# Kernel optimization log

Measured on AMD Instinct MI355X. Metric: run time of the kernel, lower is better.

The kernel has to match this reference:

```python
import jax, jax.numpy as jnp
import numpy as np

D_MODEL = 512
D_STATE = 16
D_CONV = 4
EXPAND = 2
D_INNER = EXPAND * D_MODEL          # 1024
DT_RANK = (D_MODEL + 15) // 16      # 32
B, L = 32, 2048
EPS = 1e-12


def _ln(x, g, b):
    mu = jnp.mean(x, axis=-1, keepdims=True)
    var = jnp.mean(jnp.square(x - mu), axis=-1, keepdims=True)
    return (x - mu) * jax.lax.rsqrt(var + EPS) * g + b


def setup_inputs() -> dict:
    key = jax.random.key(0)
    ks = jax.random.split(key, 12)
    s = lambda fan: 1.0 / np.sqrt(fan)
    inp = {
        "input_tensor": jax.random.normal(ks[0], (B, L, D_MODEL), jnp.float32),
        # Mamba params
        "in_proj_w": jax.random.normal(ks[1], (2 * D_INNER, D_MODEL), jnp.float32) * s(D_MODEL),
        "conv_w": jax.random.normal(ks[2], (D_INNER, D_CONV), jnp.float32) * s(D_CONV),
        "conv_b": jnp.zeros((D_INNER,), jnp.float32),
        "x_proj_w": jax.random.normal(ks[3], (DT_RANK + 2 * D_STATE, D_INNER), jnp.float32) * s(D_INNER),
        "dt_proj_w": jax.random.normal(ks[4], (D_INNER, DT_RANK), jnp.float32) * s(DT_RANK),
        "dt_proj_b": jnp.full((D_INNER,), -4.0, jnp.float32),  # softplus(-4) ~ small dt
        "A_log": jnp.log(jnp.broadcast_to(jnp.arange(1, D_STATE + 1, dtype=jnp.float32), (D_INNER, D_STATE))),
        "D": jnp.ones((D_INNER,), jnp.float32),
        "out_proj_w": jax.random.normal(ks[5], (D_MODEL, D_INNER), jnp.float32) * s(D_INNER),
        # block params
        "ln1_g": jnp.ones((D_MODEL,), jnp.float32),
        "ln1_b": jnp.zeros((D_MODEL,), jnp.float32),
        "w1_w": jax.random.normal(ks[6], (4 * D_MODEL, D_MODEL), jnp.float32) * s(D_MODEL),
        "w1_b": jnp.zeros((4 * D_MODEL,), jnp.float32),
        "w2_w": jax.random.normal(ks[7], (D_MODEL, 4 * D_MODEL), jnp.float32) * s(4 * D_MODEL),
        "w2_b": jnp.zeros((D_MODEL,), jnp.float32),
        "ln2_g": jnp.ones((D_MODEL,), jnp.float32),
        "ln2_b": jnp.zeros((D_MODEL,), jnp.float32),
    }
    return inp


def _mamba(x, in_proj_w, conv_w, conv_b, x_proj_w, dt_proj_w, dt_proj_b, A_log, D, out_proj_w):
    # x: [B, L, d_model]
    xz = jnp.einsum("bld,ed->ble", x, in_proj_w)          # [B,L,2*d_inner]
    xi, z = jnp.split(xz, 2, axis=-1)                      # each [B,L,d_inner]

    # depthwise causal conv1d along L (d_conv taps)
    xpad = jnp.pad(xi, ((0, 0), (D_CONV - 1, 0), (0, 0)))
    conv = conv_b
    for k in range(D_CONV):
        conv = conv + xpad[:, k:k + L, :] * conv_w[:, k]
    u = jax.nn.silu(conv)                                  # [B,L,d_inner]

    # input-dependent dt, B, C
    x_dbl = jnp.einsum("bld,ed->ble", u, x_proj_w)         # [B,L,dt_rank+2N]
    dt, B_t, C_t = jnp.split(x_dbl, [DT_RANK, DT_RANK + D_STATE], axis=-1)
    delta = jax.nn.softplus(jnp.einsum("blr,dr->bld", dt, dt_proj_w) + dt_proj_b)  # [B,L,d_inner]

    A = -jnp.exp(A_log)                                    # [d_inner, N]

    def step(h, inp):
        u_t, d_t, Bt, Ct = inp                             # [B,d_in],[B,d_in],[B,N],[B,N]
        dA = jnp.exp(d_t[..., None] * A)                   # [B,d_in,N]
        h = h * dA + (d_t * u_t)[..., None] * Bt[:, None, :]
        y = jnp.sum(h * Ct[:, None, :], axis=-1)           # [B,d_in]
        return h, y

    h0 = jnp.zeros((B, D_INNER, D_STATE), u.dtype)
    xs = (jnp.swapaxes(u, 0, 1), jnp.swapaxes(delta, 0, 1),
          jnp.swapaxes(B_t, 0, 1), jnp.swapaxes(C_t, 0, 1))
    _, ys = jax.lax.scan(step, h0, xs)                     # [L,B,d_inner]
    y = jnp.swapaxes(ys, 0, 1) + u * D
    y = y * jax.nn.silu(z)
    return jnp.einsum("ble,de->bld", y, out_proj_w)        # [B,L,d_model]


def reference(input_tensor, in_proj_w, conv_w, conv_b, x_proj_w, dt_proj_w, dt_proj_b,
              A_log, D, out_proj_w, ln1_g, ln1_b, w1_w, w1_b, w2_w, w2_b, ln2_g, ln2_b):
    h = _mamba(input_tensor, in_proj_w, conv_w, conv_b, x_proj_w, dt_proj_w,
               dt_proj_b, A_log, D, out_proj_w)
    h = _ln(h + input_tensor, ln1_g, ln1_b)                # num_layers > 1 branch, dropout=0
    f = jax.nn.gelu(jnp.einsum("bld,fd->blf", h, w1_w) + w1_b, approximate=False)
    f = jnp.einsum("blf,df->bld", f, w2_w) + w2_b
    return _ln(f + h, ln2_g, ln2_b)
```

## Files before the change

kernel.cpp:

```cpp
#include <hip/hip_runtime.h>
#include <hip/hip_bf16.h>

#define DM 512
#define DI 1024
#define DC 4
#define DTR 32
#define NST 16
#define LSEQ 2048
#define NBATCH 32
#define NCH 16
#define CHL 128

typedef __attribute__((ext_vector_type(8))) short b16x8;
typedef __attribute__((ext_vector_type(4))) float fx4;
typedef __attribute__((ext_vector_type(4))) unsigned short u16x4;

__device__ __forceinline__ unsigned short f2bf(float f) {
    union { float f; unsigned u; } x; x.f = f;
    unsigned r = x.u + 0x7fffu + ((x.u >> 16) & 1u);
    return (unsigned short)(r >> 16);
}
__device__ __forceinline__ float bf2f(unsigned short u) {
    union { unsigned u; float f; } x; x.u = ((unsigned)u) << 16;
    return x.f;
}

__global__ __launch_bounds__(256) void cast_kernel(const float* __restrict__ src,
                                                   unsigned short* __restrict__ dst, int n4) {
    int i = blockIdx.x * 256 + threadIdx.x;
    if (i < n4) {
        fx4 v = *(const fx4*)&src[(size_t)i * 4];
        u16x4 o;
        #pragma unroll
        for (int j = 0; j < 4; j++) o[j] = f2bf(v[j]);
        *(u16x4*)&dst[(size_t)i * 4] = o;
    }
}

__global__ __launch_bounds__(256) void extract_dt_kernel(const float* __restrict__ xdbl,
                                                         unsigned short* __restrict__ dt16) {
    int i = blockIdx.x * 256 + threadIdx.x;
    int m = i >> 5, r = i & 31;
    dt16[i] = f2bf(xdbl[(size_t)m * 64 + r]);
}

template <int BN, int EPI, bool HAS_BIAS>
__global__ __launch_bounds__(256, 2) void gemm_bf16(const unsigned short* __restrict__ A,
                                                    const unsigned short* __restrict__ W,
                                                    const float* __restrict__ bias,
                                                    void* __restrict__ Cout, int N, int K) {
    constexpr int BM = 128, BK = 32;
    __shared__ __align__(16) unsigned short As[BM * BK];
    __shared__ __align__(16) unsigned short Ws[BN * BK];
    const int tid = threadIdx.x;
    const int wave = tid >> 6, lane = tid & 63;
    const int lr = lane & 15, lg = lane >> 4;
    const int m0 = blockIdx.y * BM, n0 = blockIdx.x * BN;
    const int wm0 = (wave >> 1) * 64, wn0 = (wave & 1) * (BN / 2);
    constexpr int NR = BN / 32;
    fx4 acc[4][NR];
    #pragma unroll
    for (int i = 0; i < 4; i++)
        #pragma unroll
        for (int j = 0; j < NR; j++) acc[i][j] = fx4{0.f, 0.f, 0.f, 0.f};

    for (int k0 = 0; k0 < K; k0 += BK) {
        #pragma unroll
        for (int i = 0; i < (BM * BK / 8) / 256; i++) {
            int cb = (i * 4 + wave) * 64, c = cb + lane;
            int row = c >> 2, kk = (c & 3) * 8;
            const unsigned short* g = A + (size_t)(m0 + row) * K + k0 + kk;
            __builtin_amdgcn_global_load_lds(
                (const __attribute__((address_space(1))) unsigned int*)g,
                (__attribute__((address_space(3))) unsigned int*)&As[cb * 8], 16, 0, 0);
        }
        #pragma unroll
        for (int i = 0; i < (BN * BK / 8) / 256; i++) {
            int cb = (i * 4 + wave) * 64, c = cb + lane;
            int row = c >> 2, kk = (c & 3) * 8;
            const unsigned short* g = W + (size_t)(n0 + row) * K + k0 + kk;
            __builtin_amdgcn_global_load_lds(
                (const __attribute__((address_space(1))) unsigned int*)g,
                (__attribute__((address_space(3))) unsigned int*)&Ws[cb * 8], 16, 0, 0);
        }
        __syncthreads();
        b16x8 af[4], bfr[NR];
        #pragma unroll
        for (int mi = 0; mi < 4; mi++)
            af[mi] = *(const b16x8*)&As[(wm0 + mi * 16 + lr) * BK + lg * 8];
        #pragma unroll
        for (int ni = 0; ni < NR; ni++)
            bfr[ni] = *(const b16x8*)&Ws[(wn0 + ni * 16 + lr) * BK + lg * 8];
        #pragma unroll
        for (int mi = 0; mi < 4; mi++)
            #pragma unroll
            for (int ni = 0; ni < NR; ni++)
                acc[mi][ni] = __builtin_amdgcn_mfma_f32_16x16x32_bf16(af[mi], bfr[ni],
                                                                     acc[mi][ni], 0, 0, 0);
        __syncthreads();
    }
    #pragma unroll
    for (int mi = 0; mi < 4; mi++) {
        #pragma unroll
        for (int ni = 0; ni < NR; ni++) {
            #pragma unroll
            for (int j2 = 0; j2 < 4; j2++) {
                int row = m0 + wm0 + mi * 16 + lg * 4 + j2;
                int col = n0 + wn0 + ni * 16 + lr;
                float v = acc[mi][ni][j2];
                if (HAS_BIAS) v += bias[col];
                size_t o = (size_t)row * N + col;
                if (EPI == 0) {
                    ((float*)Cout)[o] = v;
                } else if (EPI == 1) {
                    ((unsigned short*)Cout)[o] = f2bf(v);
                } else if (EPI == 2) {
                    v = 0.5f * v * (1.f + erff(v * 0.70710678118654752f));
                    ((unsigned short*)Cout)[o] = f2bf(v);
                } else if (EPI == 3) {
                    v = (v > 20.f) ? v : log1pf(__expf(v));
                    ((float*)Cout)[o] = v;
                } else {
                    v = (v > 20.f) ? v : log1pf(__expf(v));
                    ((unsigned short*)Cout)[o] = f2bf(v);
                }
            }
        }
    }
}

__global__ __launch_bounds__(256) void conv_silu_kernel(const unsigned short* __restrict__ xz16,
                                                        const float* __restrict__ cw,
                                                        const float* __restrict__ cb,
                                                        unsigned short* __restrict__ u16) {
    int idx = blockIdx.x * 256 + threadIdx.x;
    int m = idx >> 7;
    int d0 = (idx & 127) << 3;
    int l = m & (LSEQ - 1);
    float acc[8];
    fx4 w0[8];
    #pragma unroll
    for (int j = 0; j < 8; j++) {
        acc[j] = cb[d0 + j];
        w0[j] = *(const fx4*)&cw[(d0 + j) * 4];
    }
    #pragma unroll
    for (int k = 0; k < 4; k++) {
        int lm = l - 3 + k;
        if (lm >= 0) {
            b16x8 xv = *(const b16x8*)&xz16[(size_t)(m - 3 + k) * (2 * DI) + d0];
            #pragma unroll
            for (int j = 0; j < 8; j++) acc[j] += bf2f((unsigned short)xv[j]) * w0[j][k];
        }
    }
    b16x8 o;
    #pragma unroll
    for (int j = 0; j < 8; j++) {
        float v = acc[j];
        v = v / (1.f + __expf(-v));
        o[j] = (short)f2bf(v);
    }
    *(b16x8*)&u16[(size_t)m * DI + d0] = o;
}

__device__ __forceinline__ bool load_A(const float* __restrict__ A_log, int d, float* Av) {
    bool fast = true;
    #pragma unroll
    for (int n = 0; n < NST; n++) {
        Av[n] = -__expf(A_log[(size_t)d * NST + n]);
        fast = fast && (fabsf(Av[n] + (float)(n + 1)) < 1e-4f * (float)(n + 1));
    }
    return fast;
}

__global__ __launch_bounds__(256) void scan_partial(const unsigned short* __restrict__ delta16,
                                                    const unsigned short* __restrict__ u16,
                                                    const float* __restrict__ xdbl,
                                                    const float* __restrict__ A_log,
                                                    float* __restrict__ sumd,
                                                    float* __restrict__ hend) {
    int d = blockIdx.x * 256 + threadIdx.x;
    int ch = blockIdx.y, b = blockIdx.z;
    size_t bL = (size_t)b * LSEQ + (size_t)ch * CHL;
    float Av[NST], h[NST];
    const bool fast = load_A(A_log, d, Av);
    #pragma unroll
    for (int n = 0; n < NST; n++) h[n] = 0.f;
    float S = 0.f;
    __shared__ float bs[8][16];
    for (int l0 = 0; l0 < CHL; l0 += 8) {
        __syncthreads();
        if (threadIdx.x < 128) {
            int j = threadIdx.x >> 4, c = threadIdx.x & 15;
            bs[j][c] = xdbl[(bL + l0 + j) * 64 + 32 + c];
        }
        __syncthreads();
        #pragma unroll
        for (int jj = 0; jj < 8; jj++) {
            size_t r = bL + l0 + jj;
            float dl = bf2f(delta16[r * DI + d]);
            float uu = bf2f(u16[r * DI + d]);
            S += dl;
            float du = dl * uu;
            if (fast) {
                float e1 = __expf(-dl), en = 1.f;
                #pragma unroll
                for (int n = 0; n < NST; n++) {
                    en *= e1;
                    h[n] = h[n] * en + du * bs[jj][n];
                }
            } else {
                #pragma unroll
                for (int n = 0; n < NST; n++)
                    h[n] = h[n] * __expf(dl * Av[n]) + du * bs[jj][n];
            }
        }
    }
    size_t base = ((size_t)(b * NCH + ch) * NST) * DI + d;
    #pragma unroll
    for (int n = 0; n < NST; n++) hend[base + (size_t)n * DI] = h[n];
    sumd[(size_t)(b * NCH + ch) * DI + d] = S;
}

__global__ __launch_bounds__(256) void scan_carry(const float* __restrict__ sumd,
                                                  const float* __restrict__ hend,
                                                  const float* __restrict__ A_log,
                                                  float* __restrict__ hin) {
    int d = blockIdx.x * 256 + threadIdx.x;
    int b = blockIdx.y;
    float Av[NST], h[NST];
    #pragma unroll
    for (int n = 0; n < NST; n++) {
        Av[n] = -__expf(A_log[(size_t)d * NST + n]);
        h[n] = 0.f;
    }
    for (int k = 0; k < NCH; k++) {
        size_t base = ((size_t)(b * NCH + k) * NST) * DI + d;
        float S = sumd[(size_t)(b * NCH + k) * DI + d];
        #pragma unroll
        for (int n = 0; n < NST; n++) {
            hin[base + (size_t)n * DI] = h[n];
            h[n] = h[n] * __expf(S * Av[n]) + hend[base + (size_t)n * DI];
        }
    }
}

__global__ __launch_bounds__(256) void scan_final(const unsigned short* __restrict__ delta16,
                                                  const unsigned short* u16,
                                                  const unsigned short* __restrict__ xz16,
                                                  const float* __restrict__ xdbl,
                                                  const float* __restrict__ A_log,
                                                  const float* __restrict__ Dp,
                                                  const float* __restrict__ hin,
                                                  unsigned short* y16) {
    int d = blockIdx.x * 256 + threadIdx.x;
    int ch = blockIdx.y, b = blockIdx.z;
    size_t bL = (size_t)b * LSEQ + (size_t)ch * CHL;
    float Av[NST], h[NST];
    const bool fast = load_A(A_log, d, Av);
    size_t base = ((size_t)(b * NCH + ch) * NST) * DI + d;
    #pragma unroll
    for (int n = 0; n < NST; n++) h[n] = hin[base + (size_t)n * DI];
    float Dd = Dp[d];
    __shared__ float bc[8][32];
    for (int l0 = 0; l0 < CHL; l0 += 8) {
        __syncthreads();
        {
            int j = threadIdx.x >> 5, c = threadIdx.x & 31;
            bc[j][c] = xdbl[(bL + l0 + j) * 64 + 32 + c];
        }
        __syncthreads();
        #pragma unroll
        for (int jj = 0; jj < 8; jj++) {
            size_t r = bL + l0 + jj;
            float dl = bf2f(delta16[r * DI + d]);
            float uu = bf2f(u16[r * DI + d]);
            float zz = bf2f(xz16[r * (2 * DI) + DI + d]);
            float du = dl * uu;
            float y = 0.f;
            if (fast) {
                float e1 = __expf(-dl), en = 1.f;
                #pragma unroll
                for (int n = 0; n < NST; n++) {
                    en *= e1;
                    h[n] = h[n] * en + du * bc[jj][n];
                    y += h[n] * bc[jj][16 + n];
                }
            } else {
                #pragma unroll
                for (int n = 0; n < NST; n++) {
                    h[n] = h[n] * __expf(dl * Av[n]) + du * bc[jj][n];
                    y += h[n] * bc[jj][16 + n];
                }
            }
            y = (y + uu * Dd) * (zz / (1.f + __expf(-zz)));
            y16[r * DI + d] = f2bf(y);
        }
        __syncthreads();
    }
}

__global__ __launch_bounds__(256) void ln_kernel(const float* __restrict__ a,
                                                 const float* __restrict__ res,
                                                 const float* __restrict__ g,
                                                 const float* __restrict__ bta,
                                                 float* __restrict__ out32,
                                                 unsigned short* __restrict__ out16) {
    int row = blockIdx.x, tid = threadIdx.x;
    size_t base = (size_t)row * DM;
    float v0 = a[base + tid] + res[base + tid];
    float v1 = a[base + tid + 256] + res[base + tid + 256];
    float s = v0 + v1, q = v0 * v0 + v1 * v1;
    #pragma unroll
    for (int m = 32; m >= 1; m >>= 1) {
        s += __shfl_xor(s, m);
        q += __shfl_xor(q, m);
    }
    __shared__ float rs[4], rq[4];
    int wv = tid >> 6;
    if ((tid & 63) == 0) { rs[wv] = s; rq[wv] = q; }
    __syncthreads();
    s = rs[0] + rs[1] + rs[2] + rs[3];
    q = rq[0] + rq[1] + rq[2] + rq[3];
    float mu = s * (1.f / DM);
    float var = q * (1.f / DM) - mu * mu;
    float rsg = rsqrtf(var + 1e-12f);
    float o0 = (v0 - mu) * rsg * g[tid] + bta[tid];
    float o1 = (v1 - mu) * rsg * g[tid + 256] + bta[tid + 256];
    out32[base + tid] = o0;
    out32[base + tid + 256] = o1;
    if (out16) {
        out16[base + tid] = f2bf(o0);
        out16[base + tid + 256] = f2bf(o1);
    }
}

static size_t align256(size_t b) { return (b + 255) & ~(size_t)255; }

static size_t tier_need(size_t Gb) {
    size_t R = Gb * LSEQ;
    size_t w = 0;
    w += align256((size_t)2 * DI * DM * 2);
    w += align256((size_t)64 * DI * 2);
    w += align256((size_t)DM * DI * 2);
    w += align256((size_t)4 * DM * DM * 2);
    w += align256((size_t)DM * 4 * DM * 2);
    w += align256((size_t)DI * DTR * 2);
    w += align256(R * 2048 * 2);
    w += align256(R * 1024 * 2);
    w += align256(R * 1024 * 4);
    w += align256(R * 64 * 4);
    w += align256(R * 32 * 2);
    w += align256(R * 512 * 2);
    w += align256(Gb * NCH * DI * 4);
    w += align256(Gb * NCH * NST * DI * 4);
    w += align256(Gb * NCH * NST * DI * 4);
    return w;
}

extern "C" void kernel_launch(void* const* d_in, const int* in_sizes, int n_in,
                              void* d_out, int out_size, void* d_ws, size_t ws_size,
                              hipStream_t stream) {
    const float* x_in   = (const float*)d_in[0];
    const float* inpw   = (const float*)d_in[1];
    const float* convw  = (const float*)d_in[2];
    const float* convb  = (const float*)d_in[3];
    const float* xprojw = (const float*)d_in[4];
    const float* dtw    = (const float*)d_in[5];
    const float* dtb    = (const float*)d_in[6];
    const float* A_log  = (const float*)d_in[7];
    const float* Dp     = (const float*)d_in[8];
    const float* outpw  = (const float*)d_in[9];
    const float* ln1g   = (const float*)d_in[10];
    const float* ln1b   = (const float*)d_in[11];
    const float* w1w    = (const float*)d_in[12];
    const float* w1b    = (const float*)d_in[13];
    const float* w2w    = (const float*)d_in[14];
    const float* w2b    = (const float*)d_in[15];
    const float* ln2g   = (const float*)d_in[16];
    const float* ln2b   = (const float*)d_in[17];

    int G = 1;
    const int tiers[5] = {32, 16, 8, 4, 2};
    for (int t = 0; t < 5; t++) {
        if (ws_size >= tier_need((size_t)tiers[t])) { G = tiers[t]; break; }
    }
    const size_t R = (size_t)G * LSEQ;

    char* w = (char*)d_ws;
    auto alloc = [&](size_t bytes) { char* p = w; w += align256(bytes); return p; };

    unsigned short* win16 = (unsigned short*)alloc((size_t)2 * DI * DM * 2);
    unsigned short* wxp16 = (unsigned short*)alloc((size_t)64 * DI * 2);
    unsigned short* wop16 = (unsigned short*)alloc((size_t)DM * DI * 2);
    unsigned short* ww116 = (unsigned short*)alloc((size_t)4 * DM * DM * 2);
    unsigned short* ww216 = (unsigned short*)alloc((size_t)DM * 4 * DM * 2);
    unsigned short* wdt16 = (unsigned short*)alloc((size_t)DI * DTR * 2);
    unsigned short* xz16  = (unsigned short*)alloc(R * 2048 * 2);
    unsigned short* u16   = (unsigned short*)alloc(R * 1024 * 2);
    float*          dreg  = (float*)alloc(R * 1024 * 4);
    float*          xdbl  = (float*)alloc(R * 64 * 4);
    unsigned short* dt16  = (unsigned short*)alloc(R * 32 * 2);
    unsigned short* x16   = (unsigned short*)alloc(R * 512 * 2);
    float*          sumd  = (float*)alloc((size_t)G * NCH * DI * 4);
    float*          hend  = (float*)alloc((size_t)G * NCH * NST * DI * 4);
    float*          hin   = (float*)alloc((size_t)G * NCH * NST * DI * 4);

    unsigned short* delta16 = (unsigned short*)dreg;
    unsigned short* y16 = u16;
    unsigned short* f16 = xz16;
    float*          mm32 = dreg;
    float*          h32  = dreg + R * 512;
    float*          w2o  = dreg;
    unsigned short* h16  = x16;

    dim3 blk(256);
    cast_kernel<<<(2 * DI * DM / 4 + 255) / 256, blk, 0, stream>>>(inpw, win16, 2 * DI * DM / 4);
    cast_kernel<<<(64 * DI / 4 + 255) / 256, blk, 0, stream>>>(xprojw, wxp16, 64 * DI / 4);
    cast_kernel<<<(DM * DI / 4 + 255) / 256, blk, 0, stream>>>(outpw, wop16, DM * DI / 4);
    cast_kernel<<<(4 * DM * DM / 4 + 255) / 256, blk, 0, stream>>>(w1w, ww116, 4 * DM * DM / 4);
    cast_kernel<<<(DM * 4 * DM / 4 + 255) / 256, blk, 0, stream>>>(w2w, ww216, DM * 4 * DM / 4);
    cast_kernel<<<(DI * DTR / 4 + 255) / 256, blk, 0, stream>>>(dtw, wdt16, DI * DTR / 4);

    for (int grp = 0; grp < NBATCH / G; grp++) {
        const size_t rb = (size_t)grp * R;
        const float* xg = x_in + rb * DM;
        cast_kernel<<<(int)(R * DM / 4 / 256), blk, 0, stream>>>(xg, x16, (int)(R * DM / 4));
        gemm_bf16<128, 1, false><<<dim3(2 * DI / 128, R / 128), blk, 0, stream>>>(
            x16, win16, nullptr, xz16, 2 * DI, DM);
        conv_silu_kernel<<<(int)(R * (DI / 8) / 256), blk, 0, stream>>>(xz16, convw, convb, u16);
        gemm_bf16<64, 0, false><<<dim3(1, R / 128), blk, 0, stream>>>(
            u16, wxp16, nullptr, xdbl, 64, DI);
        extract_dt_kernel<<<(int)(R * DTR / 256), blk, 0, stream>>>(xdbl, dt16);
        gemm_bf16<128, 4, true><<<dim3(DI / 128, R / 128), blk, 0, stream>>>(
            dt16, wdt16, dtb, delta16, DI, DTR);
        scan_partial<<<dim3(DI / 256, NCH, G), blk, 0, stream>>>(
            delta16, u16, xdbl, A_log, sumd, hend);
        scan_carry<<<dim3(DI / 256, G), blk, 0, stream>>>(sumd, hend, A_log, hin);
        scan_final<<<dim3(DI / 256, NCH, G), blk, 0, stream>>>(
            delta16, u16, xz16, xdbl, A_log, Dp, hin, y16);
        gemm_bf16<128, 0, false><<<dim3(DM / 128, R / 128), blk, 0, stream>>>(
            y16, wop16, nullptr, mm32, DM, DI);
        ln_kernel<<<(int)R, blk, 0, stream>>>(mm32, xg, ln1g, ln1b, h32, h16);
        gemm_bf16<128, 2, true><<<dim3(4 * DM / 128, R / 128), blk, 0, stream>>>(
            h16, ww116, w1b, f16, 4 * DM, DM);
        gemm_bf16<128, 0, true><<<dim3(DM / 128, R / 128), blk, 0, stream>>>(
            f16, ww216, w2b, w2o, DM, 4 * DM);
        ln_kernel<<<(int)R, blk, 0, stream>>>(w2o, h32, ln2g, ln2b,
                                              (float*)d_out + rb * DM, nullptr);
    }
}
```

Baseline: 1.849 ms.

## Deepen GEMM K-tile, swizzle block order, and streamline selective scan recurrence

The GEMM kernel gains a BK template parameter (64 for most calls), so each LDS stage holds two MFMA k-steps and there are half as many barriers per K. A linear block-index swizzle spreads neighbouring blocks across the grid, presumably to improve cache locality across XCDs. The scan kernels drop the shared-memory staging of B/C and its __syncthreads, reading them with vector global loads per timestep instead. They also compute the decay powers with a multiplication tree, shortening the serial multiply dependency chain. The costs are more LDS per block, which may lower occupancy, and redundant global reads of B/C by every thread.

```diff
diff --git a/kernel.cpp b/kernel.cpp
--- a/kernel.cpp
+++ b/kernel.cpp
@@ -44,18 +44,24 @@
     dt16[i] = f2bf(xdbl[(size_t)m * 64 + r]);
 }
 
-template <int BN, int EPI, bool HAS_BIAS>
+template <int BN, int BK, int EPI, bool HAS_BIAS>
 __global__ __launch_bounds__(256, 2) void gemm_bf16(const unsigned short* __restrict__ A,
                                                     const unsigned short* __restrict__ W,
                                                     const float* __restrict__ bias,
                                                     void* __restrict__ Cout, int N, int K) {
-    constexpr int BM = 128, BK = 32;
+    constexpr int BM = 128;
+    constexpr int GPR = BK / 8;
     __shared__ __align__(16) unsigned short As[BM * BK];
     __shared__ __align__(16) unsigned short Ws[BN * BK];
     const int tid = threadIdx.x;
     const int wave = tid >> 6, lane = tid & 63;
     const int lr = lane & 15, lg = lane >> 4;
-    const int m0 = blockIdx.y * BM, n0 = blockIdx.x * BN;
+    const int ntx = gridDim.x;
+    const int tot = ntx * gridDim.y;
+    const int lin = blockIdx.y * ntx + blockIdx.x;
+    const int cpx = tot >> 3;
+    const int swz = (lin & 7) * cpx + (lin >> 3);
+    const int m0 = (swz / ntx) * BM, n0 = (swz % ntx) * BN;
     const int wm0 = (wave >> 1) * 64, wn0 = (wave & 1) * (BN / 2);
     constexpr int NR = BN / 32;
     fx4 acc[4][NR];
@@ -68,7 +74,7 @@
         #pragma unroll
         for (int i = 0; i < (BM * BK / 8) / 256; i++) {
             int cb = (i * 4 + wave) * 64, c = cb + lane;
-            int row = c >> 2, kk = (c & 3) * 8;
+            int row = c / GPR, kk = (c % GPR) * 8;
             const unsigned short* g = A + (size_t)(m0 + row) * K + k0 + kk;
             __builtin_amdgcn_global_load_lds(
                 (const __attribute__((address_space(1))) unsigned int*)g,
@@ -77,26 +83,29 @@
         #pragma unroll
         for (int i = 0; i < (BN * BK / 8) / 256; i++) {
             int cb = (i * 4 + wave) * 64, c = cb + lane;
-            int row = c >> 2, kk = (c & 3) * 8;
+            int row = c / GPR, kk = (c % GPR) * 8;
             const unsigned short* g = W + (size_t)(n0 + row) * K + k0 + kk;
             __builtin_amdgcn_global_load_lds(
                 (const __attribute__((address_space(1))) unsigned int*)g,
                 (__attribute__((address_space(3))) unsigned int*)&Ws[cb * 8], 16, 0, 0);
         }
         __syncthreads();
-        b16x8 af[4], bfr[NR];
-        #pragma unroll
-        for (int mi = 0; mi < 4; mi++)
-            af[mi] = *(const b16x8*)&As[(wm0 + mi * 16 + lr) * BK + lg * 8];
-        #pragma unroll
-        for (int ni = 0; ni < NR; ni++)
-            bfr[ni] = *(const b16x8*)&Ws[(wn0 + ni * 16 + lr) * BK + lg * 8];
-        #pragma unroll
-        for (int mi = 0; mi < 4; mi++)
+        #pragma unroll
+        for (int ks = 0; ks < BK / 32; ks++) {
+            b16x8 af[4], bfr[NR];
+            #pragma unroll
+            for (int mi = 0; mi < 4; mi++)
+                af[mi] = *(const b16x8*)&As[(wm0 + mi * 16 + lr) * BK + ks * 32 + lg * 8];
             #pragma unroll
             for (int ni = 0; ni < NR; ni++)
-                acc[mi][ni] = __builtin_amdgcn_mfma_f32_16x16x32_bf16(af[mi], bfr[ni],
-                                                                     acc[mi][ni], 0, 0, 0);
+                bfr[ni] = *(const b16x8*)&Ws[(wn0 + ni * 16 + lr) * BK + ks * 32 + lg * 8];
+            #pragma unroll
+            for (int mi = 0; mi < 4; mi++)
+                #pragma unroll
+                for (int ni = 0; ni < NR; ni++)
+                    acc[mi][ni] = __builtin_amdgcn_mfma_f32_16x16x32_bf16(af[mi], bfr[ni],
+                                                                         acc[mi][ni], 0, 0, 0);
+        }
         __syncthreads();
     }
     #pragma unroll
@@ -173,6 +182,14 @@
     return fast;
 }
 
+__device__ __forceinline__ void en_tree(float e1, float* en) {
+    float e2 = e1 * e1, e3 = e2 * e1, e4 = e2 * e2, e8 = e4 * e4, e12 = e8 * e4;
+    en[0] = e1;        en[1] = e2;        en[2] = e3;        en[3] = e4;
+    en[4] = e4 * e1;   en[5] = e4 * e2;   en[6] = e4 * e3;   en[7] = e8;
+    en[8] = e8 * e1;   en[9] = e8 * e2;   en[10] = e8 * e3;  en[11] = e12;
+    en[12] = e12 * e1; en[13] = e12 * e2; en[14] = e12 * e3; en[15] = e8 * e8;
+}
+
 __global__ __launch_bounds__(256) void scan_partial(const unsigned short* __restrict__ delta16,
                                                     const unsigned short* __restrict__ u16,
                                                     const float* __restrict__ xdbl,
@@ -187,34 +204,26 @@
     #pragma unroll
     for (int n = 0; n < NST; n++) h[n] = 0.f;
     float S = 0.f;
-    __shared__ float bs[8][16];
-    for (int l0 = 0; l0 < CHL; l0 += 8) {
-        __syncthreads();
-        if (threadIdx.x < 128) {
-            int j = threadIdx.x >> 4, c = threadIdx.x & 15;
-            bs[j][c] = xdbl[(bL + l0 + j) * 64 + 32 + c];
-        }
-        __syncthreads();
-        #pragma unroll
-        for (int jj = 0; jj < 8; jj++) {
-            size_t r = bL + l0 + jj;
-            float dl = bf2f(delta16[r * DI + d]);
-            float uu = bf2f(u16[r * DI + d]);
-            S += dl;
-            float du = dl * uu;
-            if (fast) {
-                float e1 = __expf(-dl), en = 1.f;
-                #pragma unroll
-                for (int n = 0; n < NST; n++) {
-                    en *= e1;
-                    h[n] = h[n] * en + du * bs[jj][n];
-                }
-            } else {
-                #pragma unroll
-                for (int n = 0; n < NST; n++)
-                    h[n] = h[n] * __expf(dl * Av[n]) + du * bs[jj][n];
-            }
-        }
+    #pragma unroll 2
+    for (int l = 0; l < CHL; l++) {
+        size_t r = bL + l;
+        float dl = bf2f(delta16[r * DI + d]);
+        float uu = bf2f(u16[r * DI + d]);
+        S += dl;
+        float du = dl * uu;
+        const float* xr = &xdbl[r * 64 + 32];
+        float Bv[NST];
+        #pragma unroll
+        for (int t = 0; t < 4; t++) *(fx4*)&Bv[t * 4] = *(const fx4*)(xr + t * 4);
+        float en[NST];
+        if (fast) {
+            en_tree(__expf(-dl), en);
+        } else {
+            #pragma unroll
+            for (int n = 0; n < NST; n++) en[n] = __expf(dl * Av[n]);
+        }
+        #pragma unroll
+        for (int n = 0; n < NST; n++) h[n] = h[n] * en[n] + du * Bv[n];
     }
     size_t base = ((size_t)(b * NCH + ch) * NST) * DI + d;
     #pragma unroll
@@ -262,41 +271,35 @@
     #pragma unroll
     for (int n = 0; n < NST; n++) h[n] = hin[base + (size_t)n * DI];
     float Dd = Dp[d];
-    __shared__ float bc[8][32];
-    for (int l0 = 0; l0 < CHL; l0 += 8) {
-        __syncthreads();
-        {
-            int j = threadIdx.x >> 5, c = threadIdx.x & 31;
-            bc[j][c] = xdbl[(bL + l0 + j) * 64 + 32 + c];
-        }
-        __syncthreads();
-        #pragma unroll
-        for (int jj = 0; jj < 8; jj++) {
-            size_t r = bL + l0 + jj;
-            float dl = bf2f(delta16[r * DI + d]);
-            float uu = bf2f(u16[r * DI + d]);
-            float zz = bf2f(xz16[r * (2 * DI) + DI + d]);
-            float du = dl * uu;
-            float y = 0.f;
-            if (fast) {
-                float e1 = __expf(-dl), en = 1.f;
-                #pragma unroll
-                for (int n = 0; n < NST; n++) {
-                    en *= e1;
-                    h[n] = h[n] * en + du * bc[jj][n];
-                    y += h[n] * bc[jj][16 + n];
-                }
-            } else {
-                #pragma unroll
-                for (int n = 0; n < NST; n++) {
-                    h[n] = h[n] * __expf(dl * Av[n]) + du * bc[jj][n];
-                    y += h[n] * bc[jj][16 + n];
-                }
-            }
-            y = (y + uu * Dd) * (zz / (1.f + __expf(-zz)));
-            y16[r * DI + d] = f2bf(y);
-        }
-        __syncthreads();
+    #pragma unroll 2
+    for (int l = 0; l < CHL; l++) {
+        size_t r = bL + l;
+        float dl = bf2f(delta16[r * DI + d]);
+        float uu = bf2f(u16[r * DI + d]);
+        float zz = bf2f(xz16[r * (2 * DI) + DI + d]);
+        float du = dl * uu;
+        const float* xr = &xdbl[r * 64 + 32];
+        float Bv[NST], Cv[NST];
+        #pragma unroll
+        for (int t = 0; t < 4; t++) {
+            *(fx4*)&Bv[t * 4] = *(const fx4*)(xr + t * 4);
+            *(fx4*)&Cv[t * 4] = *(const fx4*)(xr + 16 + t * 4);
+        }
+        float en[NST];
+        if (fast) {
+            en_tree(__expf(-dl), en);
+        } else {
+            #pragma unroll
+            for (int n = 0; n < NST; n++) en[n] = __expf(dl * Av[n]);
+        }
+        float y = 0.f;
+        #pragma unroll
+        for (int n = 0; n < NST; n++) {
+            h[n] = h[n] * en[n] + du * Bv[n];
+            y += h[n] * Cv[n];
+        }
+        y = (y + uu * Dd) * (zz / (1.f + __expf(-zz)));
+        y16[r * DI + d] = f2bf(y);
     }
 }
 
@@ -426,25 +429,25 @@
         const size_t rb = (size_t)grp * R;
         const float* xg = x_in + rb * DM;
         cast_kernel<<<(int)(R * DM / 4 / 256), blk, 0, stream>>>(xg, x16, (int)(R * DM / 4));
-        gemm_bf16<128, 1, false><<<dim3(2 * DI / 128, R / 128), blk, 0, stream>>>(
+        gemm_bf16<128, 64, 1, false><<<dim3(2 * DI / 128, R / 128), blk, 0, stream>>>(
             x16, win16, nullptr, xz16, 2 * DI, DM);
         conv_silu_kernel<<<(int)(R * (DI / 8) / 256), blk, 0, stream>>>(xz16, convw, convb, u16);
-        gemm_bf16<64, 0, false><<<dim3(1, R / 128), blk, 0, stream>>>(
+        gemm_bf16<64, 64, 0, false><<<dim3(1, R / 128), blk, 0, stream>>>(
             u16, wxp16, nullptr, xdbl, 64, DI);
         extract_dt_kernel<<<(int)(R * DTR / 256), blk, 0, stream>>>(xdbl, dt16);
-        gemm_bf16<128, 4, true><<<dim3(DI / 128, R / 128), blk, 0, stream>>>(
+        gemm_bf16<128, 32, 4, true><<<dim3(DI / 128, R / 128), blk, 0, stream>>>(
             dt16, wdt16, dtb, delta16, DI, DTR);
         scan_partial<<<dim3(DI / 256, NCH, G), blk, 0, stream>>>(
             delta16, u16, xdbl, A_log, sumd, hend);
         scan_carry<<<dim3(DI / 256, G), blk, 0, stream>>>(sumd, hend, A_log, hin);
         scan_final<<<dim3(DI / 256, NCH, G), blk, 0, stream>>>(
             delta16, u16, xz16, xdbl, A_log, Dp, hin, y16);
-        gemm_bf16<128, 0, false><<<dim3(DM / 128, R / 128), blk, 0, stream>>>(
+        gemm_bf16<128, 64, 0, false><<<dim3(DM / 128, R / 128), blk, 0, stream>>>(
             y16, wop16, nullptr, mm32, DM, DI);
         ln_kernel<<<(int)R, blk, 0, stream>>>(mm32, xg, ln1g, ln1b, h32, h16);
-        gemm_bf16<128, 2, true><<<dim3(4 * DM / 128, R / 128), blk, 0, stream>>>(
+        gemm_bf16<128, 64, 2, true><<<dim3(4 * DM / 128, R / 128), blk, 0, stream>>>(
             h16, ww116, w1b, f16, 4 * DM, DM);
-        gemm_bf16<128, 0, true><<<dim3(DM / 128, R / 128), blk, 0, stream>>>(
+        gemm_bf16<128, 64, 0, true><<<dim3(DM / 128, R / 128), blk, 0, stream>>>(
             f16, ww216, w2b, w2o, DM, 4 * DM);
         ln_kernel<<<(int)R, blk, 0, stream>>>(w2o, h32, ln2g, ln2b,
                                               (float*)d_out + rb * DM, nullptr);
```

New measurement: 1.818 ms. Within noise of the previous version (-1.7%).
